# Performance work log

Measured on AMD Instinct MI355X. Metric: run time of the kernel, lower is better.

The kernel has to match this reference:

```python
import jax, jax.numpy as jnp
import numpy as np

N = 50000   # num nodes
D = 2       # sheaf stalk dim (final_d == d, no hp/lp)
HC = 128    # hidden channels
E0 = 200000 # undirected edges (stored in both directions -> 2*E0 directed)


def setup_inputs() -> dict:
    key = jax.random.key(0)
    k = jax.random.split(key, 6)
    x = jax.random.normal(k[0], (N * D, HC), dtype=jnp.float32)
    src = jax.random.randint(k[1], (E0,), 0, N, dtype=jnp.int32)
    dst = jax.random.randint(k[2], (E0,), 0, N, dtype=jnp.int32)
    W_sheaf = jax.random.normal(k[3], (D, 2 * D * HC), dtype=jnp.float32) * 0.05
    W_left = jax.random.normal(k[4], (D, D), dtype=jnp.float32) * 0.3
    W_right = jax.random.normal(k[5], (HC, HC), dtype=jnp.float32) * (1.0 / np.sqrt(HC))
    t = jnp.zeros((1,), dtype=jnp.float32)
    return {"t": t, "x": x, "src": src, "dst": dst,
            "W_sheaf": W_sheaf, "W_left": W_left, "W_right": W_right}


def reference(t, x, src, dst, W_sheaf, W_left, W_right):
    # Directed edge list: each undirected edge appears in both directions;
    # edge i and edge i+E0 are reverses of each other.
    row = jnp.concatenate([src, dst])  # [E]
    col = jnp.concatenate([dst, src])  # [E]
    e0 = src.shape[0]
    rev = jnp.concatenate([jnp.arange(e0) + e0, jnp.arange(e0)])

    # --- Sheaf learner (LocalConcatSheafLearner, diag maps) ---
    x_maps = x.reshape(N, D * HC)                      # node features for learner
    Wa, Wb = W_sheaf[:, : D * HC], W_sheaf[:, D * HC:]
    # tanh(Linear(cat(x_row, x_col))) without materializing the concat
    maps = jnp.tanh(x_maps[row] @ Wa.T + x_maps[col] @ Wb.T)  # [E, D]

    # --- DiagLaplacianBuilder (normalised, augmented) ---
    off = -maps * maps[rev]                                   # off-diag block (row,col): -F_e_row * F_e_col
    diag = jax.ops.segment_sum(maps ** 2, row, num_segments=N)  # [N, D]
    dis = 1.0 / jnp.sqrt(diag + 1.0)                          # augmented degree^-1/2
    off = dis[row] * off * dis[col]
    diag = dis * diag * dis

    # --- left weights: act on the d-block axis ---
    xl = (x.T.reshape(-1, D)) @ W_left.T                      # [HC*N, D]
    x = xl.reshape(HC, N * D).T                               # [N*D, HC]

    # --- right weights: act on channels ---
    x = x @ W_right.T

    # --- spmm(L, -x): block-diagonal-per-d sheaf Laplacian ---
    xb = (-x).reshape(N, D, HC)
    y = diag[..., None] * xb + jax.ops.segment_sum(off[..., None] * xb[col], row, num_segments=N)
    return y.reshape(N * D, HC)
```

## Files before the change

kernel.cpp:

```cpp
#include <hip/hip_runtime.h>

static constexpr int kN   = 50000;
static constexpr int kNR  = 100000;
static constexpr int kE0  = 200000;
static constexpr int kE2  = 400000;
static constexpr int kCAP = 32;

typedef _Float16 f16;
typedef f16   f16x8 __attribute__((ext_vector_type(8)));
typedef f16   f16x4 __attribute__((ext_vector_type(4)));
typedef float f32x4 __attribute__((ext_vector_type(4)));

__global__ __launch_bounds__(256) void k_wrh(
    const float* __restrict__ Wr, const float* __restrict__ Wsh,
    f16* __restrict__ Wrh, f16* __restrict__ Wsh8, int* __restrict__ cnt)
{
    const int i = blockIdx.x * 256 + threadIdx.x;
    if (i < kN) cnt[i] = 0;
    if (i < 16384) Wrh[i] = (f16)Wr[i];
    if (blockIdx.x == 0) {
        #pragma unroll
        for (int q = 0; q < 4; ++q) {
            const int idx = q * 256 + threadIdx.x;
            const int j = idx >> 7, k = idx & 127;
            const int srcoff = ((j >> 2) ? 256 : 0) + (((j >> 1) & 1) ? 512 : 0) + ((j & 1) ? 128 : 0);
            Wsh8[idx] = (f16)Wsh[srcoff + k];
        }
    }
}

__global__ __launch_bounds__(256) void k_node(
    const float* __restrict__ x, const float* __restrict__ Wl,
    const f16* __restrict__ Wrh, const f16* __restrict__ Wsh8,
    f16* __restrict__ xb, float* __restrict__ abf)
{
    __shared__ f16 Al[64][136];

    const int t   = threadIdx.x;
    const int blk = blockIdx.x;
    const float wl00 = Wl[0], wl01 = Wl[1], wl10 = Wl[2], wl11 = Wl[3];
    const int w = t >> 6, lane = t & 63;

    #pragma unroll
    for (int i = 0; i < 4; ++i) {
        const int f8   = i * 256 + t;
        const int row  = f8 >> 4;
        const int c8   = (f8 & 15) << 3;
        const int grow = blk * 64 + row;
        float4 xa = make_float4(0.f, 0.f, 0.f, 0.f), xc = xa;
        if (grow < kNR) {
            xa = *(const float4*)(x + (size_t)grow * 128 + c8);
            xc = *(const float4*)(x + (size_t)grow * 128 + c8 + 4);
        }
        f16x8 tv;
        tv[0] = (f16)xa.x; tv[1] = (f16)xa.y; tv[2] = (f16)xa.z; tv[3] = (f16)xa.w;
        tv[4] = (f16)xc.x; tv[5] = (f16)xc.y; tv[6] = (f16)xc.z; tv[7] = (f16)xc.w;
        *(f16x8*)&Al[row][c8] = tv;
    }
    __syncthreads();

    const int lr = lane & 15, lk = lane >> 4;

    f16x8 xfr[4], xpr[4];
    #pragma unroll
    for (int kk = 0; kk < 4; ++kk) {
        xfr[kk] = *(const f16x8*)&Al[16 * w + lr][kk * 32 + lk * 8];
        xpr[kk] = *(const f16x8*)&Al[16 * w + (lr ^ 1)][kk * 32 + lk * 8];
    }

    f32x4 cab = {0.f, 0.f, 0.f, 0.f};
    #pragma unroll
    for (int kk = 0; kk < 4; ++kk) {
        f16x8 bw = {};
        if (lr < 8) bw = *(const f16x8*)(Wsh8 + lr * 128 + kk * 32 + lk * 8);
        cab = __builtin_amdgcn_mfma_f32_16x16x32_f16(xfr[kk], bw, cab, 0, 0, 0);
    }
    #pragma unroll
    for (int tt = 0; tt < 2; ++tt) {
        const float hi_reg  = cab[2 * tt + 1];
        const float partner = __shfl_xor(hi_reg, 1);
        const float val     = cab[2 * tt] + partner;
        if (!(lr & 1) && lr < 8) {
            const int node = blk * 32 + 8 * w + 2 * lk + tt;
            if (node < kN) abf[node * 4 + (lr >> 1)] = val;
        }
    }

    const int dp = lr & 1;
    const f16 cS = (f16)(dp ? wl11 : wl00);
    const f16 cP = (f16)(dp ? wl10 : wl01);
    const f16x8 cS8 = {cS, cS, cS, cS, cS, cS, cS, cS};
    const f16x8 cP8 = {cP, cP, cP, cP, cP, cP, cP, cP};
    f16x8 tfr[4];
    #pragma unroll
    for (int kk = 0; kk < 4; ++kk)
        tfr[kk] = cS8 * xfr[kk] + cP8 * xpr[kk];

    const int grow = blk * 64 + 16 * w + lr;

    f16x8 wf0[4], wf1[4];
    #pragma unroll
    for (int kk = 0; kk < 4; ++kk)
        wf0[kk] = *(const f16x8*)(Wrh + (size_t)(0 * 16 + lr) * 128 + kk * 32 + lk * 8);

    #pragma unroll
    for (int j = 0; j < 8; ++j) {
        if (j < 7) {
            #pragma unroll
            for (int kk = 0; kk < 4; ++kk)
                wf1[kk] = *(const f16x8*)(Wrh + (size_t)((j + 1) * 16 + lr) * 128 + kk * 32 + lk * 8);
        }
        f32x4 acc = {0.f, 0.f, 0.f, 0.f};
        #pragma unroll
        for (int kk = 0; kk < 4; ++kk)
            acc = __builtin_amdgcn_mfma_f32_16x16x32_f16(wf0[kk], tfr[kk], acc, 0, 0, 0);
        f16x4 ov;
        ov[0] = (f16)(-acc[0]); ov[1] = (f16)(-acc[1]);
        ov[2] = (f16)(-acc[2]); ov[3] = (f16)(-acc[3]);
        if (grow < kNR)
            *(f16x4*)(xb + (size_t)grow * 128 + j * 16 + lk * 4) = ov;
        #pragma unroll
        for (int kk = 0; kk < 4; ++kk)
            wf0[kk] = wf1[kk];
    }
}

__global__ __launch_bounds__(256) void k_edge1(
    const int* __restrict__ src, const int* __restrict__ dst,
    const float4* __restrict__ ab, float2* __restrict__ maps2,
    int* __restrict__ cnt, int2* __restrict__ adj)
{
    const int j = blockIdx.x * 256 + threadIdx.x;
    if (j >= kE2) return;
    const bool fwd = j < kE0;
    const int o = fwd ? j : j - kE0;
    const int s = src[o], d = dst[o];
    const int row = fwd ? s : d;
    const int col = fwd ? d : s;
    const float4 ar = ab[row], ac = ab[col];
    const float m0 = tanhf(ar.x + ac.z);
    const float m1 = tanhf(ar.y + ac.w);
    maps2[j] = make_float2(m0, m1);
    const int p = atomicAdd(&cnt[row], 1);
    if (p < kCAP) adj[(size_t)row * kCAP + p] = make_int2(j, col);
}

__global__ __launch_bounds__(256) void k_diag(
    const int* __restrict__ cnt, int2* __restrict__ adj,
    const float2* __restrict__ maps2, float2* __restrict__ diag)
{
    const int node = blockIdx.x * 16 + (threadIdx.x >> 4);
    const int sl   = threadIdx.x & 15;
    if (node >= kN) return;
    int c = cnt[node];
    if (c > kCAP) c = kCAP;
    int2* al = adj + (size_t)node * kCAP;
    const int2 e0 = al[sl];
    const int2 e1 = al[sl + 16];
    float s0 = 0.f, s1 = 0.f;
    if (sl < c)      { const float2 m = maps2[e0.x]; s0 += m.x * m.x; s1 += m.y * m.y; }
    if (sl + 16 < c) { const float2 m = maps2[e1.x]; s0 += m.x * m.x; s1 += m.y * m.y; }
    const int cpad = (c + 7) & ~7;
    if (sl >= c && sl < cpad)           al[sl]      = make_int2(kE2, node);
    if (sl + 16 >= c && sl + 16 < cpad) al[sl + 16] = make_int2(kE2, node);
    #pragma unroll
    for (int o = 8; o > 0; o >>= 1) {
        s0 += __shfl_xor(s0, o);
        s1 += __shfl_xor(s1, o);
    }
    if (sl == 0) diag[node] = make_float2(s0, s1);
}

__global__ __launch_bounds__(256) void k_off(
    const int* __restrict__ src, const int* __restrict__ dst,
    const float2* __restrict__ maps2, const float2* __restrict__ diag,
    float2* __restrict__ off)
{
    const int j = blockIdx.x * 256 + threadIdx.x;
    if (j >= kE0) {
        if (j == kE0) off[kE0] = make_float2(0.f, 0.f);
        return;
    }
    const float2 ma = maps2[j];
    const float2 mb = maps2[j + kE0];
    const int s = src[j], d = dst[j];
    const float2 ds = diag[s], dt = diag[d];
    off[j] = make_float2(-ma.x * mb.x * rsqrtf((ds.x + 1.0f) * (dt.x + 1.0f)),
                         -ma.y * mb.y * rsqrtf((ds.y + 1.0f) * (dt.y + 1.0f)));
}

__global__ __launch_bounds__(256) void k_gather(
    const f16* __restrict__ xb, const float* __restrict__ diag,
    const float2* __restrict__ off, const int* __restrict__ cnt,
    const int2* __restrict__ adj, float* __restrict__ y)
{
    const int node = blockIdx.x * 4 + (threadIdx.x >> 6);
    const int lane = threadIdx.x & 63;
    const int d    = lane >> 5;
    const int h4   = (lane & 31) << 2;
    const size_t rowoff = ((size_t)node * 2 + d) * 128 + h4;
    const f16x4 own = *(const f16x4*)(xb + rowoff);
    const float dv  = diag[node * 2 + d];
    const float dg  = dv / (dv + 1.0f);
    f32x4 acc = {dg * (float)own[0], dg * (float)own[1],
                 dg * (float)own[2], dg * (float)own[3]};
    int c = cnt[node];
    if (c > kCAP) c = kCAP;
    const int2* al = adj + (size_t)node * kCAP;

    f16x4 acch = {(f16)0.f, (f16)0.f, (f16)0.f, (f16)0.f};
    for (int k = 0; k < c; k += 8) {
        const int4 ea = *(const int4*)(al + k);
        const int4 eb = *(const int4*)(al + k + 2);
        const int4 ec = *(const int4*)(al + k + 4);
        const int4 ed = *(const int4*)(al + k + 6);
        const int j0 = ea.x, n0 = ea.y, j1 = ea.z, n1 = ea.w;
        const int j2 = eb.x, n2 = eb.y, j3 = eb.z, n3 = eb.w;
        const int j4 = ec.x, n4 = ec.y, j5 = ec.z, n5 = ec.w;
        const int j6 = ed.x, n6 = ed.y, j7 = ed.z, n7 = ed.w;
        const float2 q0 = off[j0 - (j0 >= kE0 ? kE0 : 0)];
        const float2 q1 = off[j1 - (j1 >= kE0 ? kE0 : 0)];
        const float2 q2 = off[j2 - (j2 >= kE0 ? kE0 : 0)];
        const float2 q3 = off[j3 - (j3 >= kE0 ? kE0 : 0)];
        const float2 q4 = off[j4 - (j4 >= kE0 ? kE0 : 0)];
        const float2 q5 = off[j5 - (j5 >= kE0 ? kE0 : 0)];
        const float2 q6 = off[j6 - (j6 >= kE0 ? kE0 : 0)];
        const float2 q7 = off[j7 - (j7 >= kE0 ? kE0 : 0)];
        const f16x4 w0 = *(const f16x4*)(xb + ((size_t)n0 * 2 + d) * 128 + h4);
        const f16x4 w1 = *(const f16x4*)(xb + ((size_t)n1 * 2 + d) * 128 + h4);
        const f16x4 w2 = *(const f16x4*)(xb + ((size_t)n2 * 2 + d) * 128 + h4);
        const f16x4 w3 = *(const f16x4*)(xb + ((size_t)n3 * 2 + d) * 128 + h4);
        const f16x4 w4 = *(const f16x4*)(xb + ((size_t)n4 * 2 + d) * 128 + h4);
        const f16x4 w5 = *(const f16x4*)(xb + ((size_t)n5 * 2 + d) * 128 + h4);
        const f16x4 w6 = *(const f16x4*)(xb + ((size_t)n6 * 2 + d) * 128 + h4);
        const f16x4 w7 = *(const f16x4*)(xb + ((size_t)n7 * 2 + d) * 128 + h4);
        const f16 o0 = (f16)(d ? q0.y : q0.x);
        const f16 o1 = (f16)(d ? q1.y : q1.x);
        const f16 o2 = (f16)(d ? q2.y : q2.x);
        const f16 o3 = (f16)(d ? q3.y : q3.x);
        const f16 o4 = (f16)(d ? q4.y : q4.x);
        const f16 o5 = (f16)(d ? q5.y : q5.x);
        const f16 o6 = (f16)(d ? q6.y : q6.x);
        const f16 o7 = (f16)(d ? q7.y : q7.x);
        const f16x4 o40 = {o0, o0, o0, o0};
        const f16x4 o41 = {o1, o1, o1, o1};
        const f16x4 o42 = {o2, o2, o2, o2};
        const f16x4 o43 = {o3, o3, o3, o3};
        const f16x4 o44 = {o4, o4, o4, o4};
        const f16x4 o45 = {o5, o5, o5, o5};
        const f16x4 o46 = {o6, o6, o6, o6};
        const f16x4 o47 = {o7, o7, o7, o7};
        acch += o40 * w0;
        acch += o41 * w1;
        acch += o42 * w2;
        acch += o43 * w3;
        acch += o44 * w4;
        acch += o45 * w5;
        acch += o46 * w6;
        acch += o47 * w7;
    }
    acc[0] += (float)acch[0];
    acc[1] += (float)acch[1];
    acc[2] += (float)acch[2];
    acc[3] += (float)acch[3];
    __builtin_nontemporal_store(acc, (f32x4*)(y + rowoff));
}

extern "C" void kernel_launch(void* const* d_in, const int* in_sizes, int n_in,
                              void* d_out, int out_size, void* d_ws, size_t ws_size,
                              hipStream_t stream)
{
    const float* x   = (const float*)d_in[1];
    const int*   src = (const int*)d_in[2];
    const int*   dst = (const int*)d_in[3];
    const float* Wsh = (const float*)d_in[4];
    const float* Wl  = (const float*)d_in[5];
    const float* Wr  = (const float*)d_in[6];

    char* ws = (char*)d_ws;
    f16*    xb    = (f16*)   (ws + 0);
    float4* ab    = (float4*)(ws + 25600000);
    float2* maps2 = (float2*)(ws + 26400000);
    float2* off   = (float2*)(ws + 29600000);
    float2* diag  = (float2*)(ws + 31200016);
    int*    cnt   = (int*)   (ws + 31600016);
    int2*   adj   = (int2*)  (ws + 31800016);
    f16*    Wrh   = (f16*)   (ws + 44600016);
    f16*    Wsh8  = (f16*)   (ws + 44632784);

    k_wrh   <<<196,   256, 0, stream>>>(Wr, Wsh, Wrh, Wsh8, cnt);
    k_node  <<<1563,  256, 0, stream>>>(x, Wl, Wrh, Wsh8, xb, (float*)ab);
    k_edge1 <<<1563,  256, 0, stream>>>(src, dst, ab, maps2, cnt, adj);
    k_diag  <<<3125,  256, 0, stream>>>(cnt, adj, maps2, diag);
    k_off   <<<783,   256, 0, stream>>>(src, dst, maps2, diag, off);
    k_gather<<<12500, 256, 0, stream>>>(xb, (const float*)diag, off, cnt, adj, (float*)d_out);
}
```

Before: 135.0 us.

## Stage Wr in LDS for node GEMM and unroll SpMM gather to 16 edges

The node kernel now copies the f16 right-weight matrix into shared memory once per block and reads MFMA A-fragments from LDS instead of prefetching them from global memory per warp. Separately, the SpMM loop processes 16 neighbors per iteration instead of 8, with adjacency padding raised to a multiple of 16 so more independent gathers are in flight. The LDS staging adds about 35KB of shared memory per block, which may reduce occupancy. The wider unroll wastes more work on padded dummy edges for low-degree nodes (average degree is about 8).

```diff
diff --git a/kernel.cpp b/kernel.cpp
--- a/kernel.cpp
+++ b/kernel.cpp
@@ -35,11 +35,20 @@
     f16* __restrict__ xb, float* __restrict__ abf)
 {
     __shared__ f16 Al[64][136];
+    __shared__ f16 Bl[128][136];
 
     const int t   = threadIdx.x;
     const int blk = blockIdx.x;
     const float wl00 = Wl[0], wl01 = Wl[1], wl10 = Wl[2], wl11 = Wl[3];
     const int w = t >> 6, lane = t & 63;
+
+    #pragma unroll
+    for (int i = 0; i < 8; ++i) {
+        const int idx = i * 256 + t;
+        const int row = idx >> 4;
+        const int c8  = (idx & 15) << 3;
+        *(f16x8*)&Bl[row][c8] = *(const f16x8*)(Wrh + row * 128 + c8);
+    }
 
     #pragma unroll
     for (int i = 0; i < 4; ++i) {
@@ -97,31 +106,19 @@
         tfr[kk] = cS8 * xfr[kk] + cP8 * xpr[kk];
 
     const int grow = blk * 64 + 16 * w + lr;
-
-    f16x8 wf0[4], wf1[4];
-    #pragma unroll
-    for (int kk = 0; kk < 4; ++kk)
-        wf0[kk] = *(const f16x8*)(Wrh + (size_t)(0 * 16 + lr) * 128 + kk * 32 + lk * 8);
-
     #pragma unroll
     for (int j = 0; j < 8; ++j) {
-        if (j < 7) {
-            #pragma unroll
-            for (int kk = 0; kk < 4; ++kk)
-                wf1[kk] = *(const f16x8*)(Wrh + (size_t)((j + 1) * 16 + lr) * 128 + kk * 32 + lk * 8);
-        }
         f32x4 acc = {0.f, 0.f, 0.f, 0.f};
         #pragma unroll
-        for (int kk = 0; kk < 4; ++kk)
-            acc = __builtin_amdgcn_mfma_f32_16x16x32_f16(wf0[kk], tfr[kk], acc, 0, 0, 0);
+        for (int kk = 0; kk < 4; ++kk) {
+            const f16x8 wfr = *(const f16x8*)&Bl[j * 16 + lr][kk * 32 + lk * 8];
+            acc = __builtin_amdgcn_mfma_f32_16x16x32_f16(wfr, tfr[kk], acc, 0, 0, 0);
+        }
         f16x4 ov;
         ov[0] = (f16)(-acc[0]); ov[1] = (f16)(-acc[1]);
         ov[2] = (f16)(-acc[2]); ov[3] = (f16)(-acc[3]);
         if (grow < kNR)
             *(f16x4*)(xb + (size_t)grow * 128 + j * 16 + lk * 4) = ov;
-        #pragma unroll
-        for (int kk = 0; kk < 4; ++kk)
-            wf0[kk] = wf1[kk];
     }
 }
 
@@ -160,7 +157,7 @@
     float s0 = 0.f, s1 = 0.f;
     if (sl < c)      { const float2 m = maps2[e0.x]; s0 += m.x * m.x; s1 += m.y * m.y; }
     if (sl + 16 < c) { const float2 m = maps2[e1.x]; s0 += m.x * m.x; s1 += m.y * m.y; }
-    const int cpad = (c + 7) & ~7;
+    const int cpad = (c + 15) & ~15;
     if (sl >= c && sl < cpad)           al[sl]      = make_int2(kE2, node);
     if (sl + 16 >= c && sl + 16 < cpad) al[sl + 16] = make_int2(kE2, node);
     #pragma unroll
@@ -209,15 +206,23 @@
     const int2* al = adj + (size_t)node * kCAP;
 
     f16x4 acch = {(f16)0.f, (f16)0.f, (f16)0.f, (f16)0.f};
-    for (int k = 0; k < c; k += 8) {
+    for (int k = 0; k < c; k += 16) {
         const int4 ea = *(const int4*)(al + k);
         const int4 eb = *(const int4*)(al + k + 2);
         const int4 ec = *(const int4*)(al + k + 4);
         const int4 ed = *(const int4*)(al + k + 6);
-        const int j0 = ea.x, n0 = ea.y, j1 = ea.z, n1 = ea.w;
-        const int j2 = eb.x, n2 = eb.y, j3 = eb.z, n3 = eb.w;
-        const int j4 = ec.x, n4 = ec.y, j5 = ec.z, n5 = ec.w;
-        const int j6 = ed.x, n6 = ed.y, j7 = ed.z, n7 = ed.w;
+        const int4 ee = *(const int4*)(al + k + 8);
+        const int4 ef = *(const int4*)(al + k + 10);
+        const int4 eg = *(const int4*)(al + k + 12);
+        const int4 eh = *(const int4*)(al + k + 14);
+        const int j0 = ea.x,  n0 = ea.y,  j1 = ea.z,  n1 = ea.w;
+        const int j2 = eb.x,  n2 = eb.y,  j3 = eb.z,  n3 = eb.w;
+        const int j4 = ec.x,  n4 = ec.y,  j5 = ec.z,  n5 = ec.w;
+        const int j6 = ed.x,  n6 = ed.y,  j7 = ed.z,  n7 = ed.w;
+        const int j8 = ee.x,  n8 = ee.y,  j9 = ee.z,  n9 = ee.w;
+        const int jA = ef.x,  nA = ef.y,  jB = ef.z,  nB = ef.w;
+        const int jC = eg.x,  nC = eg.y,  jD = eg.z,  nD = eg.w;
+        const int jE = eh.x,  nE = eh.y,  jF = eh.z,  nF = eh.w;
         const float2 q0 = off[j0 - (j0 >= kE0 ? kE0 : 0)];
         const float2 q1 = off[j1 - (j1 >= kE0 ? kE0 : 0)];
         const float2 q2 = off[j2 - (j2 >= kE0 ? kE0 : 0)];
@@ -226,6 +231,14 @@
         const float2 q5 = off[j5 - (j5 >= kE0 ? kE0 : 0)];
         const float2 q6 = off[j6 - (j6 >= kE0 ? kE0 : 0)];
         const float2 q7 = off[j7 - (j7 >= kE0 ? kE0 : 0)];
+        const float2 q8 = off[j8 - (j8 >= kE0 ? kE0 : 0)];
+        const float2 q9 = off[j9 - (j9 >= kE0 ? kE0 : 0)];
+        const float2 qA = off[jA - (jA >= kE0 ? kE0 : 0)];
+        const float2 qB = off[jB - (jB >= kE0 ? kE0 : 0)];
+        const float2 qC = off[jC - (jC >= kE0 ? kE0 : 0)];
+        const float2 qD = off[jD - (jD >= kE0 ? kE0 : 0)];
+        const float2 qE = off[jE - (jE >= kE0 ? kE0 : 0)];
+        const float2 qF = off[jF - (jF >= kE0 ? kE0 : 0)];
         const f16x4 w0 = *(const f16x4*)(xb + ((size_t)n0 * 2 + d) * 128 + h4);
         const f16x4 w1 = *(const f16x4*)(xb + ((size_t)n1 * 2 + d) * 128 + h4);
         const f16x4 w2 = *(const f16x4*)(xb + ((size_t)n2 * 2 + d) * 128 + h4);
@@ -234,6 +247,14 @@
         const f16x4 w5 = *(const f16x4*)(xb + ((size_t)n5 * 2 + d) * 128 + h4);
         const f16x4 w6 = *(const f16x4*)(xb + ((size_t)n6 * 2 + d) * 128 + h4);
         const f16x4 w7 = *(const f16x4*)(xb + ((size_t)n7 * 2 + d) * 128 + h4);
+        const f16x4 w8 = *(const f16x4*)(xb + ((size_t)n8 * 2 + d) * 128 + h4);
+        const f16x4 w9 = *(const f16x4*)(xb + ((size_t)n9 * 2 + d) * 128 + h4);
+        const f16x4 wA = *(const f16x4*)(xb + ((size_t)nA * 2 + d) * 128 + h4);
+        const f16x4 wB = *(const f16x4*)(xb + ((size_t)nB * 2 + d) * 128 + h4);
+        const f16x4 wC = *(const f16x4*)(xb + ((size_t)nC * 2 + d) * 128 + h4);
+        const f16x4 wD = *(const f16x4*)(xb + ((size_t)nD * 2 + d) * 128 + h4);
+        const f16x4 wE = *(const f16x4*)(xb + ((size_t)nE * 2 + d) * 128 + h4);
+        const f16x4 wF = *(const f16x4*)(xb + ((size_t)nF * 2 + d) * 128 + h4);
         const f16 o0 = (f16)(d ? q0.y : q0.x);
         const f16 o1 = (f16)(d ? q1.y : q1.x);
         const f16 o2 = (f16)(d ? q2.y : q2.x);
@@ -242,22 +263,30 @@
         const f16 o5 = (f16)(d ? q5.y : q5.x);
         const f16 o6 = (f16)(d ? q6.y : q6.x);
         const f16 o7 = (f16)(d ? q7.y : q7.x);
-        const f16x4 o40 = {o0, o0, o0, o0};
-        const f16x4 o41 = {o1, o1, o1, o1};
-        const f16x4 o42 = {o2, o2, o2, o2};
-        const f16x4 o43 = {o3, o3, o3, o3};
-        const f16x4 o44 = {o4, o4, o4, o4};
-        const f16x4 o45 = {o5, o5, o5, o5};
-        const f16x4 o46 = {o6, o6, o6, o6};
-        const f16x4 o47 = {o7, o7, o7, o7};
-        acch += o40 * w0;
-        acch += o41 * w1;
-        acch += o42 * w2;
-        acch += o43 * w3;
-        acch += o44 * w4;
-        acch += o45 * w5;
-        acch += o46 * w6;
-        acch += o47 * w7;
+        const f16 o8 = (f16)(d ? q8.y : q8.x);
+        const f16 o9 = (f16)(d ? q9.y : q9.x);
+        const f16 oA = (f16)(d ? qA.y : qA.x);
+        const f16 oB = (f16)(d ? qB.y : qB.x);
+        const f16 oC = (f16)(d ? qC.y : qC.x);
+        const f16 oD = (f16)(d ? qD.y : qD.x);
+        const f16 oE = (f16)(d ? qE.y : qE.x);
+        const f16 oF = (f16)(d ? qF.y : qF.x);
+        const f16x4 o40 = {o0, o0, o0, o0};  acch += o40 * w0;
+        const f16x4 o41 = {o1, o1, o1, o1};  acch += o41 * w1;
+        const f16x4 o42 = {o2, o2, o2, o2};  acch += o42 * w2;
+        const f16x4 o43 = {o3, o3, o3, o3};  acch += o43 * w3;
+        const f16x4 o44 = {o4, o4, o4, o4};  acch += o44 * w4;
+        const f16x4 o45 = {o5, o5, o5, o5};  acch += o45 * w5;
+        const f16x4 o46 = {o6, o6, o6, o6};  acch += o46 * w6;
+        const f16x4 o47 = {o7, o7, o7, o7};  acch += o47 * w7;
+        const f16x4 o48 = {o8, o8, o8, o8};  acch += o48 * w8;
+        const f16x4 o49 = {o9, o9, o9, o9};  acch += o49 * w9;
+        const f16x4 o4A = {oA, oA, oA, oA};  acch += o4A * wA;
+        const f16x4 o4B = {oB, oB, oB, oB};  acch += o4B * wB;
+        const f16x4 o4C = {oC, oC, oC, oC};  acch += o4C * wC;
+        const f16x4 o4D = {oD, oD, oD, oD};  acch += o4D * wD;
+        const f16x4 o4E = {oE, oE, oE, oE};  acch += o4E * wE;
+        const f16x4 o4F = {oF, oF, oF, oF};  acch += o4F * wF;
     }
     acc[0] += (float)acch[0];
     acc[1] += (float)acch[1];
```

Result: slower. 143.4 us (+6.2%).
